# Kernel tuning notes

Measured on AMD Instinct MI355X. Metric: run time of the kernel, lower is better.

Reference implementation:

```python
import jax, jax.numpy as jnp
import numpy as np

B, N, E, A, H, F, HEADS = 2, 16384, 262144, 3, 128, 16, 4
DH = H // HEADS
CONST = (2.0 * np.pi) ** 0.5


def setup_inputs() -> dict:
    key = jax.random.key(0)
    ks = jax.random.split(key, 16)
    s = 0.05
    return {
        "x": jax.random.normal(ks[0], (B, N, H), jnp.float32),
        "edge_index": jax.random.randint(ks[1], (2, E), 0, N),
        # per-action message MLPs (self.mlp)
        "mlp_W1": jax.random.normal(ks[2], (A, H, H), jnp.float32) * s,
        "mlp_b1": jnp.zeros((A, H), jnp.float32),
        "mlp_W2": jax.random.normal(ks[3], (A, H, H), jnp.float32) * s,
        "mlp_b2": jnp.zeros((A, H), jnp.float32),
        # transformer (MMTs) projections, 4 heads over the action axis
        "Wq": jax.random.normal(ks[4], (H, H), jnp.float32) * s,
        "bq": jnp.zeros((H,), jnp.float32),
        "Wk": jax.random.normal(ks[5], (H, H), jnp.float32) * s,
        "bk": jnp.zeros((H,), jnp.float32),
        "Wv": jax.random.normal(ks[6], (H, H), jnp.float32) * s,
        "bv": jnp.zeros((H,), jnp.float32),
        "Wo": jax.random.normal(ks[7], (H, H), jnp.float32) * s,
        "bo": jnp.zeros((H,), jnp.float32),
        # decide_mu MLPs (decide_In_sigma is never used in the original forward)
        "mu_W1": jax.random.normal(ks[8], (A, H, H), jnp.float32) * s,
        "mu_b1": jnp.zeros((A, H), jnp.float32),
        "mu_W2": jax.random.normal(ks[9], (A, H, F), jnp.float32) * s,
        "mu_b2": jnp.zeros((A, F), jnp.float32),
    }


def _forward(x, edge_index, mlp_W1, mlp_b1, mlp_W2, mlp_b2,
             Wq, bq, Wk, bk, Wv, bv, Wo, bo, mu_W1, mu_b1, mu_W2, mu_b2):
    # per-action MLP stack: (B,N,H) -> (B,N,A,H)
    h = jax.nn.relu(jnp.einsum('bnh,ahk->bnak', x, mlp_W1) + mlp_b1)
    h = jnp.einsum('bnak,akh->bnah', h, mlp_W2) + mlp_b2
    # gather along source nodes, scatter-add into destination bins
    dst, src = edge_index[0], edge_index[1]
    g = h[:, src]                                   # (B,E,A,H) ~ 800 MB
    agg = jax.ops.segment_sum(jnp.moveaxis(g, 1, 0), dst, num_segments=N)
    agg = jnp.moveaxis(agg, 0, 1)                   # (B,N,A,H)
    # multi-head self-attention over the action axis (len A) per node
    q = (jnp.einsum('bnah,hk->bnak', agg, Wq) + bq).reshape(B, N, A, HEADS, DH)
    k = (jnp.einsum('bnah,hk->bnak', agg, Wk) + bk).reshape(B, N, A, HEADS, DH)
    v = (jnp.einsum('bnah,hk->bnak', agg, Wv) + bv).reshape(B, N, A, HEADS, DH)
    scores = jnp.einsum('bnqed,bnked->bneqk', q, k) / (DH ** 0.5)
    attn = jax.nn.softmax(scores, axis=-1)
    o = jnp.einsum('bneqk,bnked->bnqed', attn, v).reshape(B, N, A, H)
    h_I = agg + jnp.einsum('bnah,hk->bnak', o, Wo) + bo  # residual
    # per-action decode to action means: (B,N,A,F)
    m = jax.nn.relu(jnp.einsum('bnah,ahk->bnak', h_I, mu_W1) + mu_b1)
    mu = jnp.einsum('bnak,akf->bnaf', m, mu_W2) + mu_b2
    # Gaussian reparameterized sampling, VAR is a non-trainable all-ones buffer
    VAR = jnp.ones((N, A, F), jnp.float32)
    noise = jax.random.normal(jax.random.key(42), mu.shape, mu.dtype)
    sample = mu + noise * VAR
    logp = -jnp.log(CONST * VAR) - (sample - mu) ** 2 / (2.0 * VAR ** 2)
    a0 = jax.nn.softmax(jnp.tanh(sample[:, :, 0, :]), axis=-1)
    a1 = jax.nn.sigmoid(sample[:, :, 1, :])
    a2 = jnp.tanh(sample[:, :, 2, :])
    sample_out = jnp.stack([a0, a1, a2], axis=2)    # (B,N,A,F)
    return sample_out, logp.sum((-1, -2))           # ((B,N,A,F),(B,N))


def reference(x, edge_index, mlp_W1, mlp_b1, mlp_W2, mlp_b2,
              Wq, bq, Wk, bk, Wv, bv, Wo, bo, mu_W1, mu_b1, mu_W2, mu_b2):
    return _forward(x, edge_index, mlp_W1, mlp_b1, mlp_W2, mlp_b2,
                    Wq, bq, Wk, bk, Wv, bv, Wo, bo, mu_W1, mu_b1, mu_W2, mu_b2)
```

## Files before the change

### kernel.cpp

```cpp
#include <hip/hip_runtime.h>
#include <hip/hip_bf16.h>

#define NN    16384
#define EE    262144
#define BNODES 32768
#define AH    384
#define TOT_NOISE 1572864u

typedef __attribute__((ext_vector_type(8))) short short8;
typedef __attribute__((ext_vector_type(4))) float v4f;

__device__ __forceinline__ unsigned short f2bf(float f) {
  unsigned u = __float_as_uint(f);
  unsigned r = u + 0x7fffu + ((u >> 16) & 1u);
  return (unsigned short)(r >> 16);
}
__device__ __forceinline__ float bf2f(unsigned short h) {
  return __uint_as_float(((unsigned)h) << 16);
}
__device__ __forceinline__ float bflo(unsigned u) { return __uint_as_float(u << 16); }
__device__ __forceinline__ float bfhi(unsigned u) { return __uint_as_float(u & 0xffff0000u); }
__device__ __forceinline__ unsigned pk_bf16(float a, float b) {
  __hip_bfloat162 h = __float22bfloat162_rn(make_float2(a, b));
  return *(unsigned*)&h;
}

__device__ __forceinline__ void threefry2x32_042(unsigned& x0, unsigned& x1) {
  const unsigned ks0 = 0u;
  const unsigned ks1 = 42u;
  const unsigned ks2 = 0x1BD11BDAu ^ 0u ^ 42u;
  x0 += ks0; x1 += ks1;
#define TFR(r) { x0 += x1; x1 = (x1 << (r)) | (x1 >> (32 - (r))); x1 ^= x0; }
  TFR(13) TFR(15) TFR(26) TFR(6)   x0 += ks1; x1 += ks2 + 1u;
  TFR(17) TFR(29) TFR(16) TFR(24)  x0 += ks2; x1 += ks0 + 2u;
  TFR(13) TFR(15) TFR(26) TFR(6)   x0 += ks0; x1 += ks1 + 3u;
  TFR(17) TFR(29) TFR(16) TFR(24)  x0 += ks1; x1 += ks2 + 4u;
  TFR(13) TFR(15) TFR(26) TFR(6)   x0 += ks2; x1 += ks0 + 5u;
#undef TFR
}

__device__ __forceinline__ float erfinv_f32(float x) {
  float w = -log1pf(-x * x);
  float p;
  if (w < 5.0f) {
    w -= 2.5f;
    p = 2.81022636e-08f;
    p = fmaf(p, w, 3.43273939e-07f);
    p = fmaf(p, w, -3.5233877e-06f);
    p = fmaf(p, w, -4.39150654e-06f);
    p = fmaf(p, w, 0.00021858087f);
    p = fmaf(p, w, -0.00125372503f);
    p = fmaf(p, w, -0.00417768164f);
    p = fmaf(p, w, 0.246640727f);
    p = fmaf(p, w, 1.50140941f);
  } else {
    w = sqrtf(w) - 3.0f;
    p = -0.000200214257f;
    p = fmaf(p, w, 0.000100950558f);
    p = fmaf(p, w, 0.00134934322f);
    p = fmaf(p, w, -0.00367342844f);
    p = fmaf(p, w, 0.00573950773f);
    p = fmaf(p, w, -0.0076224613f);
    p = fmaf(p, w, 0.00943887047f);
    p = fmaf(p, w, 1.00167406f);
    p = fmaf(p, w, 2.83297682f);
  }
  return p * x;
}

__device__ __forceinline__ unsigned jax_random_bits32(unsigned i) {
  unsigned x0 = 0u, x1 = i;
  threefry2x32_042(x0, x1);
  return x0 ^ x1;
}

__device__ __forceinline__ float jax_normal_from_bits(unsigned bits) {
  float f = __uint_as_float((bits >> 9) | 0x3f800000u) - 1.0f;
  const float lo = -0.99999994f;
  float u = f * 2.0f + lo;
  u = fmaxf(u, lo);
  return 1.4142135623730951f * erfinv_f32(u);
}

__global__ void edge_count(const int* __restrict__ dst, int* __restrict__ deg) {
  int e = blockIdx.x * 256 + threadIdx.x;
  if (e < EE) atomicAdd(&deg[dst[e]], 1);
}

__global__ __launch_bounds__(1024) void scan_k(const int* __restrict__ deg,
                                               int* __restrict__ offs,
                                               int* __restrict__ cur) {
  __shared__ int wsum[16];
  const int t = threadIdx.x;
  const int base = t * 16;
  int loc[16];
  int s = 0;
#pragma unroll
  for (int i = 0; i < 16; i++) { loc[i] = deg[base + i]; s += loc[i]; }
  const int mysum = s;
  const int lane = t & 63, wid = t >> 6;
#pragma unroll
  for (int off = 1; off < 64; off <<= 1) {
    int v = __shfl_up(s, off, 64);
    if (lane >= off) s += v;
  }
  if (lane == 63) wsum[wid] = s;
  __syncthreads();
  if (t == 0) {
    int r = 0;
#pragma unroll
    for (int i = 0; i < 16; i++) { int v = wsum[i]; wsum[i] = r; r += v; }
  }
  __syncthreads();
  int run = wsum[wid] + s - mysum;
#pragma unroll
  for (int i = 0; i < 16; i++) {
    offs[base + i] = run;
    cur[base + i] = run;
    run += loc[i];
  }
  if (t == 1023) offs[NN] = run;
}

__global__ void edge_fill(const int* __restrict__ dst, const int* __restrict__ srcv,
                          int* __restrict__ cur, int* __restrict__ csr) {
  int e = blockIdx.x * 256 + threadIdx.x;
  if (e < EE) {
    int d = dst[e];
    int p = atomicAdd(&cur[d], 1);
    csr[p] = srcv[e];
  }
}

__global__ __launch_bounds__(256) void prep_wfrag(
    const float* __restrict__ W1, const float* __restrict__ W2,
    const float* __restrict__ mW1,
    const float* __restrict__ Wq, const float* __restrict__ Wk,
    const float* __restrict__ Wv, const float* __restrict__ Wo,
    const float* __restrict__ mW2,
    unsigned short* __restrict__ F) {
  int m = blockIdx.y;
  int f = blockIdx.x * 256 + threadIdx.x;
  if (m == 13) {
    if (f < 6144) {
      int a = f >> 11;
      int r2 = f & 2047;
      int kt = r2 >> 9;
      int r = r2 & 511;
      int lane = r >> 3, j = r & 7;
      int k = kt * 32 + (lane >> 4) * 8 + j;
      int n = lane & 15;
      F[13 * 16384 + f] = f2bf(mW2[(a * 128 + k) * 16 + n]);
    }
    return;
  }
  const float* W;
  if (m < 3) W = W1 + (long)m * 16384;
  else if (m < 6) W = W2 + (long)(m - 3) * 16384;
  else if (m < 9) W = mW1 + (long)(m - 6) * 16384;
  else W = (m == 9) ? Wq : (m == 10) ? Wk : (m == 11) ? Wv : Wo;
  int tile = f >> 9;
  int kt = tile >> 3, nt = tile & 7;
  int r = f & 511;
  int lane = r >> 3, j = r & 7;
  int k = kt * 32 + (lane >> 4) * 8 + j;
  int n = nt * 16 + (lane & 15);
  F[(long)m * 16384 + f] = f2bf(W[k * 128 + n]);
}

#define GXSTR 136
__global__ __launch_bounds__(256, 4) void mlp_fused(
    const float* __restrict__ X,
    const unsigned short* __restrict__ WF1, const float* __restrict__ b1,
    const unsigned short* __restrict__ WF2, const float* __restrict__ b2,
    unsigned short* __restrict__ H) {
  __shared__ __align__(16) unsigned short As[128 * GXSTR];
  const int a = blockIdx.y;
  const long m0 = (long)blockIdx.x * 128;
  const int tid = threadIdx.x;
  const unsigned short* Wp1 = WF1 + (long)a * 16384;
  const unsigned short* Wp2 = WF2 + (long)a * 16384;

#pragma unroll
  for (int p = 0; p < 8; p++) {
    int c = tid + p * 256;
    int row = c >> 4, c8 = (c & 15) * 8;
    float4 v1 = *(const float4*)(X + (m0 + row) * 128 + c8);
    float4 v2 = *(const float4*)(X + (m0 + row) * 128 + c8 + 4);
    uint4 o = make_uint4(pk_bf16(v1.x, v1.y), pk_bf16(v1.z, v1.w),
                         pk_bf16(v2.x, v2.y), pk_bf16(v2.z, v2.w));
    *(uint4*)(&As[row * GXSTR + c8]) = o;
  }
  __syncthreads();

  const int w = tid >> 6, l = tid & 63, lr = l & 15, lg = l >> 4;

  v4f acc[8][2];
#pragma unroll
  for (int mt = 0; mt < 8; mt++) {
    acc[mt][0] = (v4f){0.f, 0.f, 0.f, 0.f};
    acc[mt][1] = (v4f){0.f, 0.f, 0.f, 0.f};
  }
#pragma unroll
  for (int kt = 0; kt < 4; kt++) {
    short8 bfr[2];
#pragma unroll
    for (int ntl = 0; ntl < 2; ntl++)
      bfr[ntl] = *(const short8*)(Wp1 + (long)(kt * 8 + 2 * w + ntl) * 512 + l * 8);
#pragma unroll
    for (int mt = 0; mt < 8; mt++) {
      short8 af = *(const short8*)(&As[(mt * 16 + lr) * GXSTR + kt * 32 + lg * 8]);
      acc[mt][0] = __builtin_amdgcn_mfma_f32_16x16x32_bf16(af, bfr[0], acc[mt][0], 0, 0, 0);
      acc[mt][1] = __builtin_amdgcn_mfma_f32_16x16x32_bf16(af, bfr[1], acc[mt][1], 0, 0, 0);
    }
  }
  __syncthreads();

  {
    float bv[2] = {b1[a * 128 + 32 * w + lr], b1[a * 128 + 32 * w + 16 + lr]};
#pragma unroll
    for (int mt = 0; mt < 8; mt++)
#pragma unroll
      for (int ntl = 0; ntl < 2; ntl++)
#pragma unroll
        for (int i = 0; i < 4; i++) {
          int row = mt * 16 + lg * 4 + i;
          int col = 32 * w + ntl * 16 + lr;
          As[row * GXSTR + col] = f2bf(fmaxf(acc[mt][ntl][i] + bv[ntl], 0.0f));
        }
  }
  __syncthreads();

#pragma unroll
  for (int mt = 0; mt < 8; mt++) {
    acc[mt][0] = (v4f){0.f, 0.f, 0.f, 0.f};
    acc[mt][1] = (v4f){0.f, 0.f, 0.f, 0.f};
  }
#pragma unroll
  for (int kt = 0; kt < 4; kt++) {
    short8 bfr[2];
#pragma unroll
    for (int ntl = 0; ntl < 2; ntl++)
      bfr[ntl] = *(const short8*)(Wp2 + (long)(kt * 8 + 2 * w + ntl) * 512 + l * 8);
#pragma unroll
    for (int mt = 0; mt < 8; mt++) {
      short8 af = *(const short8*)(&As[(mt * 16 + lr) * GXSTR + kt * 32 + lg * 8]);
      acc[mt][0] = __builtin_amdgcn_mfma_f32_16x16x32_bf16(af, bfr[0], acc[mt][0], 0, 0, 0);
      acc[mt][1] = __builtin_amdgcn_mfma_f32_16x16x32_bf16(af, bfr[1], acc[mt][1], 0, 0, 0);
    }
  }
  {
    float bv[2] = {b2[a * 128 + 32 * w + lr], b2[a * 128 + 32 * w + 16 + lr]};
#pragma unroll
    for (int mt = 0; mt < 8; mt++)
#pragma unroll
      for (int ntl = 0; ntl < 2; ntl++)
#pragma unroll
        for (int i = 0; i < 4; i++) {
          long row = m0 + mt * 16 + lg * 4 + i;
          int col = 32 * w + ntl * 16 + lr;
          H[row * 384 + a * 128 + col] = f2bf(acc[mt][ntl][i] + bv[ntl]);
        }
  }
}

#define XSTR 136
#define QSTR 34
__global__ __launch_bounds__(256, 3) void attn_mega(
    const unsigned short* __restrict__ H, const int* __restrict__ offs,
    const int* __restrict__ csr,
    const unsigned short* __restrict__ WF,
    const float* __restrict__ bq, const float* __restrict__ bk,
    const float* __restrict__ bv, const float* __restrict__ bo,
    const unsigned short* __restrict__ WM1, const float* __restrict__ mb1,
    const unsigned short* __restrict__ WM2, const float* __restrict__ mb2,
    float* __restrict__ out0, float* __restrict__ out1) {
  __shared__ __align__(16) unsigned short xS[48 * XSTR];
  __shared__ __align__(16) unsigned short kS[4 * 48 * QSTR];
  __shared__ __align__(16) unsigned short vS[4 * 48 * QSTR];
  __shared__ float lpS[48];

  const int tid = threadIdx.x;
  const long node0 = (long)blockIdx.x * 16;

  {
    const int bt = (int)(node0 >> 14);
    const int nbase = (int)(node0 & (NN - 1));
    const int nd = tid >> 4;
    const int sub = tid & 15;
    const int n = nbase + nd;
    const int e0 = offs[n], e1 = offs[n + 1];
    const unsigned short* hb = H + (long)bt * NN * 384 + sub * 24;
    float acc24[24];
#pragma unroll
    for (int i = 0; i < 24; i++) acc24[i] = 0.f;

#define ACC8(base, u)                                                   \
    { acc24[base+0] += bflo(u.x); acc24[base+1] += bfhi(u.x);           \
      acc24[base+2] += bflo(u.y); acc24[base+3] += bfhi(u.y);           \
      acc24[base+4] += bflo(u.z); acc24[base+5] += bfhi(u.z);           \
      acc24[base+6] += bflo(u.w); acc24[base+7] += bfhi(u.w); }
#define LDPAIR(B0,B1,B2,B3,B4,B5, jj)                                   \
    { int s0 = csr[jj], s1 = csr[(jj) + 1];                             \
      const unsigned short* p0 = hb + (long)s0 * 384;                   \
      const unsigned short* p1 = hb + (long)s1 * 384;                   \
      B0 = *(const uint4*)(p0);  B1 = *(const uint4*)(p0 + 8);          \
      B2 = *(const uint4*)(p0 + 16);                                    \
      B3 = *(const uint4*)(p1);  B4 = *(const uint4*)(p1 + 8);          \
      B5 = *(const uint4*)(p1 + 16); }
#define ACCP(B0,B1,B2,B3,B4,B5)                                         \
    { ACC8(0,B0) ACC8(8,B1) ACC8(16,B2) ACC8(0,B3) ACC8(8,B4) ACC8(16,B5) }

    const int npair = (e1 - e0) >> 1;
    int j = e0;
    if (npair > 0) {
      uint4 a0, a1, a2, a3, a4, a5;
      uint4 b0, b1, b2, b3, b4, b5;
      LDPAIR(a0, a1, a2, a3, a4, a5, j);
      int g = 0;
      while (true) {
        if (g + 1 < npair) {
          LDPAIR(b0, b1, b2, b3, b4, b5, j + 2);
          ACCP(a0, a1, a2, a3, a4, a5);
          g++; j += 2;
          if (g + 1 < npair) {
            LDPAIR(a0, a1, a2, a3, a4, a5, j + 2);
            ACCP(b0, b1, b2, b3, b4, b5);
            g++; j += 2;
          } else {
            ACCP(b0, b1, b2, b3, b4, b5);
            g++; j += 2;
            break;
          }
        } else {
          ACCP(a0, a1, a2, a3, a4, a5);
          g++; j += 2;
          break;
        }
      }
    }
    if (j < e1) {
      int s0 = csr[j];
      const unsigned short* p0 = hb + (long)s0 * 384;
      uint4 A0 = *(const uint4*)(p0);
      uint4 A1 = *(const uint4*)(p0 + 8);
      uint4 A2 = *(const uint4*)(p0 + 16);
      ACC8(0, A0) ACC8(8, A1) ACC8(16, A2)
    }
#undef ACCP
#undef LDPAIR
#undef ACC8
#pragma unroll
    for (int jj = 0; jj < 12; jj++) {
      int g = sub * 24 + 2 * jj;
      int a_ = g >> 7;
      int c = g & 127;
      *(unsigned*)&xS[(3 * nd + a_) * XSTR + c] =
          pk_bf16(acc24[2 * jj], acc24[2 * jj + 1]);
    }
  }
  __syncthreads();

  const int w = tid >> 6;
  const int l = tid & 63;
  const int lr = l & 15;
  const int lg = l >> 4;
  const unsigned short* WQ = WF;
  const unsigned short* WK = WF + 16384;
  const unsigned short* WV = WF + 32768;
  const unsigned short* WO = WF + 49152;

  v4f accq[3][2], acck[3][2], accv[3][2];
#pragma unroll
  for (int mt = 0; mt < 3; mt++)
#pragma unroll
    for (int n = 0; n < 2; n++) {
      accq[mt][n] = (v4f){0.f, 0.f, 0.f, 0.f};
      acck[mt][n] = (v4f){0.f, 0.f, 0.f, 0.f};
      accv[mt][n] = (v4f){0.f, 0.f, 0.f, 0.f};
    }
#pragma unroll
  for (int kt = 0; kt < 4; kt++) {
    short8 af[3];
#pragma unroll
    for (int mt = 0; mt < 3; mt++)
      af[mt] = *(const short8*)&xS[(mt * 16 + lr) * XSTR + kt * 32 + lg * 8];
#pragma unroll
    for (int ntl = 0; ntl < 2; ntl++) {
      long tf = (long)(kt * 8 + 2 * w + ntl) * 512 + l * 8;
      short8 b0 = *(const short8*)&WQ[tf];
      short8 b1 = *(const short8*)&WK[tf];
      short8 b2 = *(const short8*)&WV[tf];
#pragma unroll
      for (int mt = 0; mt < 3; mt++) {
        accq[mt][ntl] = __builtin_amdgcn_mfma_f32_16x16x32_bf16(af[mt], b0, accq[mt][ntl], 0, 0, 0);
        acck[mt][ntl] = __builtin_amdgcn_mfma_f32_16x16x32_bf16(af[mt], b1, acck[mt][ntl], 0, 0, 0);
        accv[mt][ntl] = __builtin_amdgcn_mfma_f32_16x16x32_bf16(af[mt], b2, accv[mt][ntl], 0, 0, 0);
      }
    }
  }
  __syncthreads();

  float resv[3][2][4];
#pragma unroll
  for (int mt = 0; mt < 3; mt++)
#pragma unroll
    for (int ntl = 0; ntl < 2; ntl++)
#pragma unroll
      for (int i = 0; i < 4; i++)
        resv[mt][ntl][i] =
            bf2f(xS[(mt * 16 + lg * 4 + i) * XSTR + 32 * w + ntl * 16 + lr]);

  {
    const float scale = 0.17677669529663687f;
    unsigned short* kw = &kS[w * 48 * QSTR];
    unsigned short* vw = &vS[w * 48 * QSTR];
    float bqv[2] = {bq[32 * w + lr], bq[32 * w + 16 + lr]};
    float bkv[2] = {bk[32 * w + lr], bk[32 * w + 16 + lr]};
    float bvv[2] = {bv[32 * w + lr], bv[32 * w + 16 + lr]};
#pragma unroll
    for (int mt = 0; mt < 3; mt++)
#pragma unroll
      for (int ntl = 0; ntl < 2; ntl++)
#pragma unroll
        for (int i = 0; i < 4; i++) {
          int row = mt * 16 + lg * 4 + i;
          int col = ntl * 16 + lr;
          xS[row * XSTR + 32 * w + col] = f2bf((accq[mt][ntl][i] + bqv[ntl]) * scale);
          kw[row * QSTR + col] = f2bf(acck[mt][ntl][i] + bkv[ntl]);
          vw[row * QSTR + col] = f2bf(accv[mt][ntl][i] + bvv[ntl]);
        }
  }
  __syncthreads();

  if (l < 48) {
    int aq = l % 3;
    int ndr = l - aq;
    const unsigned* qr = (const unsigned*)&xS[l * XSTR + 32 * w];
    const unsigned* kr0 = (const unsigned*)&kS[(w * 48 + ndr) * QSTR];
    const unsigned* kr1 = (const unsigned*)&kS[(w * 48 + ndr + 1) * QSTR];
    const unsigned* kr2 = (const unsigned*)&kS[(w * 48 + ndr + 2) * QSTR];
    float s0 = 0.f, s1 = 0.f, s2 = 0.f;
#pragma unroll
    for (int j = 0; j < 16; j++) {
      unsigned uq = qr[j], u0 = kr0[j], u1 = kr1[j], u2 = kr2[j];
      float qa = bflo(uq), qb = bfhi(uq);
      s0 = fmaf(qa, bflo(u0), fmaf(qb, bfhi(u0), s0));
      s1 = fmaf(qa, bflo(u1), fmaf(qb, bfhi(u1), s1));
      s2 = fmaf(qa, bflo(u2), fmaf(qb, bfhi(u2), s2));
    }
    float mx = fmaxf(s0, fmaxf(s1, s2));
    float e0 = expf(s0 - mx), e1 = expf(s1 - mx), e2 = expf(s2 - mx);
    float inv = 1.0f / (e0 + e1 + e2);
    e0 *= inv; e1 *= inv; e2 *= inv;
    const unsigned* vr0 = (const unsigned*)&vS[(w * 48 + ndr) * QSTR];
    const unsigned* vr1 = (const unsigned*)&vS[(w * 48 + ndr + 1) * QSTR];
    const unsigned* vr2 = (const unsigned*)&vS[(w * 48 + ndr + 2) * QSTR];
    unsigned ov[16];
#pragma unroll
    for (int j = 0; j < 16; j++) {
      unsigned u0 = vr0[j], u1 = vr1[j], u2 = vr2[j];
      float oa = fmaf(e0, bflo(u0), fmaf(e1, bflo(u1), e2 * bflo(u2)));
      float ob = fmaf(e0, bfhi(u0), fmaf(e1, bfhi(u1), e2 * bfhi(u2)));
      ov[j] = pk_bf16(oa, ob);
    }
    uint4* orow = (uint4*)&xS[l * XSTR + 32 * w];
    orow[0] = make_uint4(ov[0], ov[1], ov[2], ov[3]);
    orow[1] = make_uint4(ov[4], ov[5], ov[6], ov[7]);
    orow[2] = make_uint4(ov[8], ov[9], ov[10], ov[11]);
    orow[3] = make_uint4(ov[12], ov[13], ov[14], ov[15]);
  }
  __syncthreads();

  v4f acco[3][2];
#pragma unroll
  for (int mt = 0; mt < 3; mt++)
#pragma unroll
    for (int n = 0; n < 2; n++) acco[mt][n] = (v4f){0.f, 0.f, 0.f, 0.f};
#pragma unroll
  for (int kt = 0; kt < 4; kt++) {
    short8 af[3];
#pragma unroll
    for (int mt = 0; mt < 3; mt++)
      af[mt] = *(const short8*)&xS[(mt * 16 + lr) * XSTR + kt * 32 + lg * 8];
#pragma unroll
    for (int ntl = 0; ntl < 2; ntl++) {
      long tf = (long)(kt * 8 + 2 * w + ntl) * 512 + l * 8;
      short8 b = *(const short8*)&WO[tf];
#pragma unroll
      for (int mt = 0; mt < 3; mt++)
        acco[mt][ntl] = __builtin_amdgcn_mfma_f32_16x16x32_bf16(af[mt], b, acco[mt][ntl], 0, 0, 0);
    }
  }
  __syncthreads();

  {
    float bov[2] = {bo[32 * w + lr], bo[32 * w + 16 + lr]};
#pragma unroll
    for (int mt = 0; mt < 3; mt++)
#pragma unroll
      for (int ntl = 0; ntl < 2; ntl++)
#pragma unroll
        for (int i = 0; i < 4; i++) {
          int row = mt * 16 + lg * 4 + i;
          int nd = row / 3, a_ = row - nd * 3;
          int gcol = 32 * w + ntl * 16 + lr;
          xS[(a_ * 16 + nd) * XSTR + gcol] =
              f2bf(acco[mt][ntl][i] + bov[ntl] + resv[mt][ntl][i]);
        }
  }
  __syncthreads();

  v4f accm[3][2];
#pragma unroll
  for (int mt = 0; mt < 3; mt++)
#pragma unroll
    for (int n = 0; n < 2; n++) accm[mt][n] = (v4f){0.f, 0.f, 0.f, 0.f};
#pragma unroll
  for (int kt = 0; kt < 4; kt++) {
#pragma unroll
    for (int mt = 0; mt < 3; mt++) {
      short8 af = *(const short8*)&xS[(mt * 16 + lr) * XSTR + kt * 32 + lg * 8];
#pragma unroll
      for (int ntl = 0; ntl < 2; ntl++) {
        short8 b = *(const short8*)(WM1 + (long)mt * 16384 +
                                    (long)(kt * 8 + 2 * w + ntl) * 512 + l * 8);
        accm[mt][ntl] = __builtin_amdgcn_mfma_f32_16x16x32_bf16(af, b, accm[mt][ntl], 0, 0, 0);
      }
    }
  }
  __syncthreads();

#pragma unroll
  for (int mt = 0; mt < 3; mt++)
#pragma unroll
    for (int ntl = 0; ntl < 2; ntl++) {
      int col = 32 * w + ntl * 16 + lr;
      float bias = mb1[mt * 128 + col];
#pragma unroll
      for (int i = 0; i < 4; i++) {
        int rowp = mt * 16 + lg * 4 + i;
        xS[rowp * XSTR + col] = f2bf(fmaxf(accm[mt][ntl][i] + bias, 0.0f));
      }
    }
  __syncthreads();

  if (w < 3) {
    v4f accu = (v4f){0.f, 0.f, 0.f, 0.f};
#pragma unroll
    for (int kt = 0; kt < 4; kt++) {
      short8 af = *(const short8*)&xS[(w * 16 + lr) * XSTR + kt * 32 + lg * 8];
      short8 b = *(const short8*)(WM2 + w * 2048 + kt * 512 + l * 8);
      accu = __builtin_amdgcn_mfma_f32_16x16x32_bf16(af, b, accu, 0, 0, 0);
    }
    float bias = mb2[w * 16 + lr];
#pragma unroll
    for (int i = 0; i < 4; i++) {
      int nd = lg * 4 + i;
      float mu = accu[i] + bias;
      unsigned gidx = (unsigned)((node0 + nd) * 48 + w * 16 + lr);
      unsigned bits = jax_random_bits32(gidx);
      float noise = jax_normal_from_bits(bits);
      float sample = mu + noise;
      float lp = -0.9189385332046727f - 0.5f * noise * noise;
      lp += __shfl_xor(lp, 1, 64);
      lp += __shfl_xor(lp, 2, 64);
      lp += __shfl_xor(lp, 4, 64);
      lp += __shfl_xor(lp, 8, 64);
      if (lr == 0) lpS[w * 16 + nd] = lp;
      float res;
      if (w == 0) {
        float th = tanhf(sample);
        float mx = th;
        mx = fmaxf(mx, __shfl_xor(mx, 1, 64));
        mx = fmaxf(mx, __shfl_xor(mx, 2, 64));
        mx = fmaxf(mx, __shfl_xor(mx, 4, 64));
        mx = fmaxf(mx, __shfl_xor(mx, 8, 64));
        float ex = expf(th - mx);
        float ss = ex;
        ss += __shfl_xor(ss, 1, 64);
        ss += __shfl_xor(ss, 2, 64);
        ss += __shfl_xor(ss, 4, 64);
        ss += __shfl_xor(ss, 8, 64);
        res = ex / ss;
      } else if (w == 1) {
        res = 1.0f / (1.0f + expf(-sample));
      } else {
        res = tanhf(sample);
      }
      out0[gidx] = res;
    }
  }
  __syncthreads();
  if (tid < 16)
    out1[node0 + tid] = lpS[tid] + lpS[16 + tid] + lpS[32 + tid];
}

extern "C" void kernel_launch(void* const* d_in, const int* in_sizes, int n_in,
                              void* d_out, int out_size, void* d_ws, size_t ws_size,
                              hipStream_t stream) {
  const float* x = (const float*)d_in[0];
  const int* ei = (const int*)d_in[1];
  const float* W1 = (const float*)d_in[2];
  const float* b1 = (const float*)d_in[3];
  const float* W2 = (const float*)d_in[4];
  const float* b2 = (const float*)d_in[5];
  const float* Wq = (const float*)d_in[6];
  const float* bq = (const float*)d_in[7];
  const float* Wk = (const float*)d_in[8];
  const float* bk = (const float*)d_in[9];
  const float* Wv = (const float*)d_in[10];
  const float* bv = (const float*)d_in[11];
  const float* Wo = (const float*)d_in[12];
  const float* bo = (const float*)d_in[13];
  const float* mW1 = (const float*)d_in[14];
  const float* mb1 = (const float*)d_in[15];
  const float* mW2 = (const float*)d_in[16];
  const float* mb2 = (const float*)d_in[17];
  (void)in_sizes; (void)n_in; (void)out_size; (void)ws_size;

  unsigned short* HB = (unsigned short*)d_ws;
  int* deg = (int*)(HB + 12582912);
  int* offs = deg + NN;
  int* cur = offs + (NN + 1);
  int* csr = cur + NN;
  unsigned short* wfrag = (unsigned short*)(((uintptr_t)(csr + EE) + 15) & ~(uintptr_t)15);
  unsigned short* w2frag = wfrag + 13 * 16384;

  const int* dst = ei;
  const int* srcv = ei + EE;

  float* out0 = (float*)d_out;
  float* out1 = out0 + TOT_NOISE;

  hipMemsetAsync(deg, 0, NN * sizeof(int), stream);
  edge_count<<<EE / 256, 256, 0, stream>>>(dst, deg);
  scan_k<<<1, 1024, 0, stream>>>(deg, offs, cur);
  edge_fill<<<EE / 256, 256, 0, stream>>>(dst, srcv, cur, csr);
  prep_wfrag<<<dim3(64, 14), 256, 0, stream>>>(W1, W2, mW1, Wq, Wk, Wv, Wo, mW2, wfrag);

  mlp_fused<<<dim3(BNODES / 128, 3), 256, 0, stream>>>(x, wfrag, b1, wfrag + 3 * 16384, b2, HB);
  attn_mega<<<BNODES / 16, 256, 0, stream>>>(HB, offs, csr,
                                             wfrag + 9 * 16384, bq, bk, bv, bo,
                                             wfrag + 6 * 16384, mb1, w2frag, mb2,
                                             out0, out1);
}
```

Measured before the change: 231.6 us.

## Pipeline CSR gather with swizzle-broadcast indices and 4-deep row prefetch

Rewrites the neighbor aggregation loop so the 16 lanes serving one node cooperatively load 16 CSR indices at once and broadcast them with ds_swizzle. A rotating set of four row buffers keeps three gathers in flight ahead of accumulation. This replaces serial per-edge index loads and two-deep pairing, aiming to hide more gather latency. It also raises the launch-bounds occupancy hint from 3 to 4 blocks, which may force register spills given the larger buffer set.

```diff
diff --git a/kernel.cpp b/kernel.cpp
--- a/kernel.cpp
+++ b/kernel.cpp
@@ -266,7 +266,7 @@
 
 #define XSTR 136
 #define QSTR 34
-__global__ __launch_bounds__(256, 3) void attn_mega(
+__global__ __launch_bounds__(256, 4) void attn_mega(
     const unsigned short* __restrict__ H, const int* __restrict__ offs,
     const int* __restrict__ csr,
     const unsigned short* __restrict__ WF,
@@ -290,6 +290,7 @@
     const int sub = tid & 15;
     const int n = nbase + nd;
     const int e0 = offs[n], e1 = offs[n + 1];
+    const int cnt = e1 - e0;
     const unsigned short* hb = H + (long)bt * NN * 384 + sub * 24;
     float acc24[24];
 #pragma unroll
@@ -300,55 +301,74 @@
       acc24[base+2] += bflo(u.y); acc24[base+3] += bfhi(u.y);           \
       acc24[base+4] += bflo(u.z); acc24[base+5] += bfhi(u.z);           \
       acc24[base+6] += bflo(u.w); acc24[base+7] += bfhi(u.w); }
-#define LDPAIR(B0,B1,B2,B3,B4,B5, jj)                                   \
-    { int s0 = csr[jj], s1 = csr[(jj) + 1];                             \
-      const unsigned short* p0 = hb + (long)s0 * 384;                   \
-      const unsigned short* p1 = hb + (long)s1 * 384;                   \
-      B0 = *(const uint4*)(p0);  B1 = *(const uint4*)(p0 + 8);          \
-      B2 = *(const uint4*)(p0 + 16);                                    \
-      B3 = *(const uint4*)(p1);  B4 = *(const uint4*)(p1 + 8);          \
-      B5 = *(const uint4*)(p1 + 16); }
-#define ACCP(B0,B1,B2,B3,B4,B5)                                         \
-    { ACC8(0,B0) ACC8(8,B1) ACC8(16,B2) ACC8(0,B3) ACC8(8,B4) ACC8(16,B5) }
-
-    const int npair = (e1 - e0) >> 1;
-    int j = e0;
-    if (npair > 0) {
-      uint4 a0, a1, a2, a3, a4, a5;
-      uint4 b0, b1, b2, b3, b4, b5;
-      LDPAIR(a0, a1, a2, a3, a4, a5, j);
-      int g = 0;
-      while (true) {
-        if (g + 1 < npair) {
-          LDPAIR(b0, b1, b2, b3, b4, b5, j + 2);
-          ACCP(a0, a1, a2, a3, a4, a5);
-          g++; j += 2;
-          if (g + 1 < npair) {
-            LDPAIR(a0, a1, a2, a3, a4, a5, j + 2);
-            ACCP(b0, b1, b2, b3, b4, b5);
-            g++; j += 2;
-          } else {
-            ACCP(b0, b1, b2, b3, b4, b5);
-            g++; j += 2;
-            break;
-          }
-        } else {
-          ACCP(a0, a1, a2, a3, a4, a5);
-          g++; j += 2;
-          break;
-        }
-      }
-    }
-    if (j < e1) {
-      int s0 = csr[j];
-      const unsigned short* p0 = hb + (long)s0 * 384;
-      uint4 A0 = *(const uint4*)(p0);
-      uint4 A1 = *(const uint4*)(p0 + 8);
-      uint4 A2 = *(const uint4*)(p0 + 16);
-      ACC8(0, A0) ACC8(8, A1) ACC8(16, A2)
-    }
-#undef ACCP
-#undef LDPAIR
+#define GACC(BUF, KK)                                                   \
+    if ((KK) < cnt) { ACC8(0, BUF##0) ACC8(8, BUF##1) ACC8(16, BUF##2) }
+#define ROWLD(BUF, SPTR)                                                \
+    { const unsigned short* p_ = hb + (long)(SPTR) * 384;               \
+      BUF##0 = *(const uint4*)(p_);                                     \
+      BUF##1 = *(const uint4*)(p_ + 8);                                 \
+      BUF##2 = *(const uint4*)(p_ + 16); }
+
+    int ai0 = e0 + sub;        ai0 = (ai0 < EE) ? ai0 : (EE - 1);
+    int ai1 = e0 + 16 + sub;   ai1 = (ai1 < EE) ? ai1 : (EE - 1);
+    int idx_cur = csr[ai0];
+    int idx_nxt = csr[ai1];
+
+    uint4 A0, A1, A2, B0, B1, B2, C0, C1, C2, D0, D1, D2;
+    {
+      int t0 = (0 < cnt) ? __builtin_amdgcn_ds_swizzle(idx_cur, (0 << 5) | 16) : 0;
+      int t1 = (1 < cnt) ? __builtin_amdgcn_ds_swizzle(idx_cur, (1 << 5) | 16) : 0;
+      int t2 = (2 < cnt) ? __builtin_amdgcn_ds_swizzle(idx_cur, (2 << 5) | 16) : 0;
+      ROWLD(A, t0)
+      ROWLD(B, t1)
+      ROWLD(C, t2)
+    }
+
+    int j = 0;
+    while (j < cnt) {
+      int idx_fut;
+      { int a2 = e0 + j + 32 + sub; a2 = (a2 < EE) ? a2 : (EE - 1); idx_fut = csr[a2]; }
+      int sv[16];
+      sv[0]  = (j + 3  < cnt) ? __builtin_amdgcn_ds_swizzle(idx_cur, (3  << 5) | 16) : 0;
+      sv[1]  = (j + 4  < cnt) ? __builtin_amdgcn_ds_swizzle(idx_cur, (4  << 5) | 16) : 0;
+      sv[2]  = (j + 5  < cnt) ? __builtin_amdgcn_ds_swizzle(idx_cur, (5  << 5) | 16) : 0;
+      sv[3]  = (j + 6  < cnt) ? __builtin_amdgcn_ds_swizzle(idx_cur, (6  << 5) | 16) : 0;
+      sv[4]  = (j + 7  < cnt) ? __builtin_amdgcn_ds_swizzle(idx_cur, (7  << 5) | 16) : 0;
+      sv[5]  = (j + 8  < cnt) ? __builtin_amdgcn_ds_swizzle(idx_cur, (8  << 5) | 16) : 0;
+      sv[6]  = (j + 9  < cnt) ? __builtin_amdgcn_ds_swizzle(idx_cur, (9  << 5) | 16) : 0;
+      sv[7]  = (j + 10 < cnt) ? __builtin_amdgcn_ds_swizzle(idx_cur, (10 << 5) | 16) : 0;
+      sv[8]  = (j + 11 < cnt) ? __builtin_amdgcn_ds_swizzle(idx_cur, (11 << 5) | 16) : 0;
+      sv[9]  = (j + 12 < cnt) ? __builtin_amdgcn_ds_swizzle(idx_cur, (12 << 5) | 16) : 0;
+      sv[10] = (j + 13 < cnt) ? __builtin_amdgcn_ds_swizzle(idx_cur, (13 << 5) | 16) : 0;
+      sv[11] = (j + 14 < cnt) ? __builtin_amdgcn_ds_swizzle(idx_cur, (14 << 5) | 16) : 0;
+      sv[12] = (j + 15 < cnt) ? __builtin_amdgcn_ds_swizzle(idx_cur, (15 << 5) | 16) : 0;
+      sv[13] = (j + 16 < cnt) ? __builtin_amdgcn_ds_swizzle(idx_nxt, (0  << 5) | 16) : 0;
+      sv[14] = (j + 17 < cnt) ? __builtin_amdgcn_ds_swizzle(idx_nxt, (1  << 5) | 16) : 0;
+      sv[15] = (j + 18 < cnt) ? __builtin_amdgcn_ds_swizzle(idx_nxt, (2  << 5) | 16) : 0;
+
+      GACC(A, j + 0)   ROWLD(D, sv[0])
+      GACC(B, j + 1)   ROWLD(A, sv[1])
+      GACC(C, j + 2)   ROWLD(B, sv[2])
+      GACC(D, j + 3)   ROWLD(C, sv[3])
+      GACC(A, j + 4)   ROWLD(D, sv[4])
+      GACC(B, j + 5)   ROWLD(A, sv[5])
+      GACC(C, j + 6)   ROWLD(B, sv[6])
+      GACC(D, j + 7)   ROWLD(C, sv[7])
+      GACC(A, j + 8)   ROWLD(D, sv[8])
+      GACC(B, j + 9)   ROWLD(A, sv[9])
+      GACC(C, j + 10)  ROWLD(B, sv[10])
+      GACC(D, j + 11)  ROWLD(C, sv[11])
+      GACC(A, j + 12)  ROWLD(D, sv[12])
+      GACC(B, j + 13)  ROWLD(A, sv[13])
+      GACC(C, j + 14)  ROWLD(B, sv[14])
+      GACC(D, j + 15)  ROWLD(C, sv[15])
+
+      idx_cur = idx_nxt;
+      idx_nxt = idx_fut;
+      j += 16;
+    }
+#undef ROWLD
+#undef GACC
 #undef ACC8
 #pragma unroll
     for (int jj = 0; jj < 12; jj++) {
```

After: 274.6 us. 1.19x slower.
